# Kernel optimization log

Hardware: AMD Instinct MI355X
Metric: run time of the kernel (lower is better)

The kernel has to match this reference:

```python
import math
import jax, jax.numpy as jnp
import numpy as np
from jax.scipy.linalg import solve_triangular

K, D, Q = 512, 2048, 8
B = 8192
EPS = 1e-5
RHO0 = math.log(math.exp(1.0) - 1.0)  # softplus^-1(1.0), matches psi_init=scale_init=1.0


def setup_inputs() -> dict:
    key = jax.random.key(0)
    k1, k2, k3, k4, k5 = jax.random.split(key, 5)
    x = jax.random.normal(k1, (B, D), dtype=jnp.float32)
    mu = jax.random.normal(k2, (K, D), dtype=jnp.float32)          # centroids
    dir_raw = jax.random.normal(k3, (K, D, Q), dtype=jnp.float32) / math.sqrt(D)
    scale_rho = jnp.full((K, Q), RHO0, dtype=jnp.float32) + 0.01 * jax.random.normal(k4, (K, Q), dtype=jnp.float32)
    psi_rho = jnp.full((D,), RHO0, dtype=jnp.float32) + 0.01 * jax.random.normal(k5, (D,), dtype=jnp.float32)
    pi_logits = jnp.zeros((K,), dtype=jnp.float32)
    return {"x": x, "mu": mu, "dir_raw": dir_raw, "scale_rho": scale_rho,
            "psi_rho": psi_rho, "pi_logits": pi_logits}


def _nll(x, mu, dir_raw, scale_rho, psi_rho, pi_logits):
    Dd = x.shape[1]
    q = dir_raw.shape[2]
    # diagonal noise (shared across components since psi_per_component=False)
    psi = jax.nn.softplus(psi_rho) + EPS                      # (D,)
    psi_inv = 1.0 / psi                                       # (D,)
    # factor loadings W_k = normalize(dir_raw, dim=1) * softplus(scale)
    n = jnp.maximum(jnp.linalg.norm(dir_raw, axis=1, keepdims=True), EPS)
    W = (dir_raw / n) * jax.nn.softplus(scale_rho)[:, None, :]  # (K, D, q)
    # Woodbury inner matrix M_k = I + W^T Psi^{-1} W and its Cholesky
    A = W * jnp.sqrt(psi_inv)[None, :, None]                  # (K, D, q)
    M = jnp.einsum('kdi,kdj->kij', A, A) + jnp.eye(q, dtype=W.dtype)[None]
    L = jnp.linalg.cholesky(M)                                # (K, q, q) lower
    # quadratic form pieces
    xT_Pinv_x = (x ** 2) @ psi_inv                            # (B,)
    xT_Pinv_mu = x @ (psi_inv[None, :] * mu).T                # (B, K)
    muT_Pinv_mu = jnp.sum(mu ** 2 * psi_inv[None, :], axis=-1)  # (K,)
    quad_Psi = xT_Pinv_x[:, None] - 2.0 * xT_Pinv_mu + muT_Pinv_mu[None, :]
    PinvW = psi_inv[None, :, None] * W                        # (K, D, q)
    WT_Pinv_x = jnp.einsum('bd,kdq->bkq', x, PinvW)           # (B, K, q)
    WT_Pinv_mu = jnp.einsum('kd,kdq->kq', mu, PinvW)          # (K, q)
    v = WT_Pinv_x - WT_Pinv_mu[None, :, :]                    # (B, K, q)
    # Ez = M^{-1} v via the Cholesky factor (batched over K, rhs over B)
    vT = jnp.transpose(v, (1, 2, 0))                          # (K, q, B)
    y = solve_triangular(L, vT, lower=True)
    EzT = solve_triangular(jnp.swapaxes(L, -1, -2), y, lower=False)
    Ez = jnp.transpose(EzT, (2, 0, 1))                        # (B, K, q)
    quad = quad_Psi - jnp.sum(v * Ez, axis=-1)                # (B, K)
    # log-determinants via Woodbury: log|C| = log|Psi| + log|M|
    logdet_Psi = jnp.sum(jnp.log(psi))                        # scalar (shared psi)
    logdet_M = 2.0 * jnp.sum(jnp.log(jnp.diagonal(L, axis1=-2, axis2=-1)), axis=-1)  # (K,)
    logdet_C = logdet_Psi + logdet_M                          # (K,)
    ll = -0.5 * (Dd * math.log(2.0 * math.pi) + logdet_C[None, :] + quad)  # (B, K)
    log_pi = jax.nn.log_softmax(pi_logits)
    logp = jax.scipy.special.logsumexp(ll + log_pi[None, :], axis=1)  # (B,)
    return jnp.mean(-logp)


def reference(x, mu, dir_raw, scale_rho, psi_rho, pi_logits):
    return _nll(x, mu, dir_raw, scale_rho, psi_rho, pi_logits)
```

## Files before the change

### kernel.cpp

```cpp
#include <hip/hip_runtime.h>

constexpr int Bn = 8192;
constexpr int Dd = 2048;
constexpr int Kk = 512;
constexpr int Qq = 8;
constexpr int Nn = Kk * 9;
constexpr float DLOG2PI = 3763.9722f;

constexpr int BM = 256, BN = 144, BK = 128;

constexpr float SX = 16.f;
constexpr float SW = 64.f;
constexpr float SG = 16.f;
constexpr float INV_UW = 1.f / (16.f * 64.f);
constexpr float INV_UG = 1.f / (16.f * 16.f);

constexpr size_t OFF_PSI   = 0;
constexpr size_t OFF_LDP   = 8192;
constexpr size_t OFF_LOGPI = 8448;
constexpr size_t OFF_OFFK  = 10752;
constexpr size_t OFF_MINV  = 13056;
constexpr size_t OFF_XPX   = 144384;
constexpr size_t OFF_XBF   = 177408;
constexpr size_t OFF_GT    = 33731840;
constexpr size_t OFF_LL    = 52606208;
constexpr size_t OFF_PART  = 69383424;

typedef float f32x4 __attribute__((ext_vector_type(4)));
typedef int   i32x4v __attribute__((ext_vector_type(4)));
typedef int   i32x8v __attribute__((ext_vector_type(8)));

__device__ inline float softplusf(float x) {
  return fmaxf(x, 0.f) + log1pf(expf(-fabsf(x)));
}
__device__ inline unsigned short f2bf(float x) {
  unsigned int u = __builtin_bit_cast(unsigned int, x);
  u = (u + 0x7fffu + ((u >> 16) & 1u)) >> 16;
  return (unsigned short)u;
}
__device__ inline unsigned int pack2(float a, float b) {
  return (unsigned int)f2bf(a) | ((unsigned int)f2bf(b) << 16);
}
__device__ inline float bf2f(unsigned int u16) {
  unsigned int v = u16 << 16;
  return __builtin_bit_cast(float, v);
}
__device__ inline unsigned char f2fp8(float x) {
  int v = __builtin_amdgcn_cvt_pk_fp8_f32(x, 0.f, 0, false);
  return (unsigned char)(v & 0xff);
}
__device__ inline void glds16(const unsigned char* g, char* l) {
  __builtin_amdgcn_global_load_lds(
      (const __attribute__((address_space(1))) unsigned int*)g,
      (__attribute__((address_space(3))) unsigned int*)l, 16, 0, 0);
}
__device__ inline i32x8v ld_frag(const char* rowp, int quad, int s8) {
  i32x4v lo = *(const i32x4v*)(rowp + (((2 * quad)     ^ s8) * 16));
  i32x4v hi = *(const i32x4v*)(rowp + (((2 * quad + 1) ^ s8) * 16));
  i32x8v r;
  r[0] = lo[0]; r[1] = lo[1]; r[2] = lo[2]; r[3] = lo[3];
  r[4] = hi[0]; r[5] = hi[1]; r[6] = hi[2]; r[7] = hi[3];
  return r;
}

__global__ __launch_bounds__(256) void prep_psi(
    const float* __restrict__ psi_rho, const float* __restrict__ pi_logits,
    float* __restrict__ psi_inv, float* __restrict__ logdetPsi,
    float* __restrict__ logpi) {
  __shared__ float red[256];
  int t = threadIdx.x;
  float acc = 0.f;
  for (int d = t; d < Dd; d += 256) {
    float p = softplusf(psi_rho[d]) + 1e-5f;
    psi_inv[d] = 1.f / p;
    acc += logf(p);
  }
  red[t] = acc;
  __syncthreads();
  for (int s = 128; s > 0; s >>= 1) { if (t < s) red[t] += red[t + s]; __syncthreads(); }
  if (t == 0) *logdetPsi = red[0];
  __syncthreads();
  float mx = -3.4e38f;
  for (int i = t; i < Kk; i += 256) mx = fmaxf(mx, pi_logits[i]);
  red[t] = mx;
  __syncthreads();
  for (int s = 128; s > 0; s >>= 1) { if (t < s) red[t] = fmaxf(red[t], red[t + s]); __syncthreads(); }
  mx = red[0];
  __syncthreads();
  float se = 0.f;
  for (int i = t; i < Kk; i += 256) se += expf(pi_logits[i] - mx);
  red[t] = se;
  __syncthreads();
  for (int s = 128; s > 0; s >>= 1) { if (t < s) red[t] += red[t + s]; __syncthreads(); }
  float lse = mx + logf(red[0]);
  for (int i = t; i < Kk; i += 256) logpi[i] = pi_logits[i] - lse;
}

__global__ __launch_bounds__(256) void prep_all(
    const float* __restrict__ x, const float* __restrict__ mu,
    const float* __restrict__ dir_raw, const float* __restrict__ scale_rho,
    const float* __restrict__ psi_inv,
    float* __restrict__ offk, float* __restrict__ Minv,
    unsigned char* __restrict__ Gq, unsigned char* __restrict__ xq,
    float* __restrict__ xPx) {
  __shared__ unsigned short sDir[Dd * 8];
  __shared__ float sPwmd[Dd];
  __shared__ float redk[4 * 53];
  __shared__ float R[53];
  __shared__ float sAl[8], sAh[8];

  int bid = blockIdx.x;
  int t = threadIdx.x, lane = t & 63, w = t >> 6;

  if (bid >= Kk) {
    int b = bid - Kk;
    const float4* xr = (const float4*)(x + (size_t)b * Dd);
    const float4* pr = (const float4*)psi_inv;
    float4 v0 = xr[2 * t], v1 = xr[2 * t + 1];
    float4 p0 = pr[2 * t], p1 = pr[2 * t + 1];
    float acc = v0.x * v0.x * p0.x + v0.y * v0.y * p0.y + v0.z * v0.z * p0.z + v0.w * v0.w * p0.w
              + v1.x * v1.x * p1.x + v1.y * v1.y * p1.y + v1.z * v1.z * p1.z + v1.w * v1.w * p1.w;
    unsigned int q0 = (unsigned int)__builtin_amdgcn_cvt_pk_fp8_f32(SX * v0.x, SX * v0.y, 0, false);
    q0 = (unsigned int)__builtin_amdgcn_cvt_pk_fp8_f32(SX * v0.z, SX * v0.w, (int)q0, true);
    unsigned int q1 = (unsigned int)__builtin_amdgcn_cvt_pk_fp8_f32(SX * v1.x, SX * v1.y, 0, false);
    q1 = (unsigned int)__builtin_amdgcn_cvt_pk_fp8_f32(SX * v1.z, SX * v1.w, (int)q1, true);
    uint2 o; o.x = q0; o.y = q1;
    *(uint2*)(xq + (size_t)b * Dd + t * 8) = o;
#pragma unroll
    for (int s2 = 32; s2; s2 >>= 1) acc += __shfl_down(acc, s2, 64);
    float* r4 = sPwmd;
    if (lane == 0) r4[w] = acc;
    __syncthreads();
    if (t == 0) xPx[b] = r4[0] + r4[1] + r4[2] + r4[3];
    return;
  }

  int k = bid;
  float vals[53];
#pragma unroll
  for (int i = 0; i < 53; i++) vals[i] = 0.f;
  const float4* dirp = (const float4*)(dir_raw + (size_t)k * Dd * Qq);
  for (int d = t; d < Dd; d += 256) {
    float4 da = dirp[d * 2], db = dirp[d * 2 + 1];
    float dir8[8] = {da.x, da.y, da.z, da.w, db.x, db.y, db.z, db.w};
    float pw = psi_inv[d];
    float md = mu[(size_t)k * Dd + d];
    int c = 0;
#pragma unroll
    for (int i = 0; i < 8; i++) {
      float dip = dir8[i] * pw;
#pragma unroll
      for (int j = 0; j < 8; j++) {
        if (j < i) continue;
        vals[c] += dip * dir8[j]; c++;
      }
    }
#pragma unroll
    for (int q = 0; q < 8; q++) vals[36 + q] += dir8[q] * dir8[q];
    float mp = md * pw;
#pragma unroll
    for (int q = 0; q < 8; q++) vals[44 + q] += mp * dir8[q];
    vals[52] += md * mp;
    uint4 pk;
    pk.x = pack2(pw * dir8[0], pw * dir8[1]);
    pk.y = pack2(pw * dir8[2], pw * dir8[3]);
    pk.z = pack2(pw * dir8[4], pw * dir8[5]);
    pk.w = pack2(pw * dir8[6], pw * dir8[7]);
    *(uint4*)(sDir + d * 8) = pk;
    sPwmd[d] = mp;
  }
#pragma unroll
  for (int v = 0; v < 53; v++) {
    float val = vals[v];
#pragma unroll
    for (int o = 32; o; o >>= 1) val += __shfl_down(val, o, 64);
    if (lane == 0) redk[w * 53 + v] = val;
  }
  __syncthreads();
  if (t < 53) R[t] = redk[t] + redk[53 + t] + redk[106 + t] + redk[159 + t];
  __syncthreads();
  if (t == 0) {
    float Sf[8][8];
    {
      int c2 = 0;
#pragma unroll
      for (int i = 0; i < 8; i++) {
#pragma unroll
        for (int j = 0; j < 8; j++) {
          if (j < i) continue;
          float v = R[c2++]; Sf[i][j] = v; Sf[j][i] = v;
        }
      }
    }
    float alpha[8];
#pragma unroll
    for (int q = 0; q < 8; q++) {
      float nr = fmaxf(sqrtf(R[36 + q]), 1e-5f);
      alpha[q] = softplusf(scale_rho[(size_t)k * 8 + q]) / nr;
    }
    float Mm[8][8];
#pragma unroll
    for (int i = 0; i < 8; i++)
#pragma unroll
      for (int j = 0; j < 8; j++)
        Mm[i][j] = alpha[i] * alpha[j] * Sf[i][j] + (i == j ? 1.f : 0.f);
    float L[8][8], Ld[8];
#pragma unroll
    for (int i = 0; i < 8; i++) {
#pragma unroll
      for (int j = 0; j < 8; j++) {
        if (j > i) continue;
        float s2 = Mm[i][j];
#pragma unroll
        for (int p = 0; p < 8; p++) { if (p < j) s2 -= L[i][p] * L[j][p]; }
        if (i == j) { L[i][i] = sqrtf(s2); Ld[i] = 1.f / L[i][i]; }
        else        L[i][j] = s2 * Ld[j];
      }
    }
    float logdetM = 0.f;
#pragma unroll
    for (int i = 0; i < 8; i++) logdetM += 2.f * logf(L[i][i]);
    float wv[8];
#pragma unroll
    for (int q = 0; q < 8; q++) wv[q] = alpha[q] * R[44 + q];
    float y[8], h[8];
#pragma unroll
    for (int i = 0; i < 8; i++) {
      float s2 = wv[i];
#pragma unroll
      for (int p = 0; p < 8; p++) { if (p < i) s2 -= L[i][p] * y[p]; }
      y[i] = s2 * Ld[i];
    }
#pragma unroll
    for (int i = 7; i >= 0; i--) {
      float s2 = y[i];
#pragma unroll
      for (int p = 0; p < 8; p++) { if (p > i) s2 -= L[p][i] * h[p]; }
      h[i] = s2 * Ld[i];
    }
    float cc = R[52];
#pragma unroll
    for (int q = 0; q < 8; q++) cc -= wv[q] * h[q];
#pragma unroll
    for (int col = 0; col < 8; col++) {
      float yy[8], z[8];
#pragma unroll
      for (int i = 0; i < 8; i++) {
        float s2 = (i == col) ? 1.f : 0.f;
#pragma unroll
        for (int p = 0; p < 8; p++) { if (p < i) s2 -= L[i][p] * yy[p]; }
        yy[i] = s2 * Ld[i];
      }
#pragma unroll
      for (int i = 7; i >= 0; i--) {
        float s2 = yy[i];
#pragma unroll
        for (int p = 0; p < 8; p++) { if (p > i) s2 -= L[p][i] * z[p]; }
        z[i] = s2 * Ld[i];
      }
#pragma unroll
      for (int r2 = 0; r2 < 8; r2++) Minv[(size_t)k * 64 + r2 * 8 + col] = z[r2];
    }
    offk[k] = -0.5f * (DLOG2PI + logdetM + cc);
#pragma unroll
    for (int q = 0; q < 8; q++) { sAl[q] = alpha[q]; sAh[q] = alpha[q] * h[q]; }
  }
  __syncthreads();
  float al[8], ah[8];
#pragma unroll
  for (int q = 0; q < 8; q++) { al[q] = sAl[q]; ah[q] = sAh[q]; }
  for (int d = t; d < Dd; d += 256) {
    uint4 pk = *(const uint4*)(sDir + d * 8);
    float pd[8];
    pd[0] = bf2f(pk.x & 0xffffu); pd[1] = bf2f(pk.x >> 16);
    pd[2] = bf2f(pk.y & 0xffffu); pd[3] = bf2f(pk.y >> 16);
    pd[4] = bf2f(pk.z & 0xffffu); pd[5] = bf2f(pk.z >> 16);
    pd[6] = bf2f(pk.w & 0xffffu); pd[7] = bf2f(pk.w >> 16);
    float gs = 0.f;
#pragma unroll
    for (int q = 0; q < 8; q++) {
      Gq[((size_t)(k * 9 + q)) * Dd + d] = f2fp8(SW * al[q] * pd[q]);
      gs += ah[q] * pd[q];
    }
    Gq[((size_t)(k * 9 + 8)) * Dd + d] = f2fp8(SG * (sPwmd[d] - gs));
  }
}

__global__ __launch_bounds__(256, 2) void gemm_ll(
    const unsigned char* __restrict__ xq, const unsigned char* __restrict__ Gq,
    const float* __restrict__ Minv, const float* __restrict__ offk,
    const float* __restrict__ logpi, const float* __restrict__ logdetPsi,
    const float* __restrict__ xPx, float* __restrict__ ll) {
  __shared__ char smem[55424];
  float* Cs    = (float*)smem;
  float* sMinv = (float*)(smem + 51200);
  float* sOff  = (float*)(smem + 51200 + 4160);

  int t = threadIdx.x, lane = t & 63, w = t >> 6;
  int m0 = blockIdx.y * BM;
  int n0 = blockIdx.x * BN;
  int comp0 = blockIdx.x * 16;

  for (int i = t; i < 1024; i += 256) {
    int cl = i >> 6, idx = i & 63;
    sMinv[cl * 65 + idx] = Minv[(size_t)comp0 * 64 + i];
  }
  if (t < 16)
    sOff[t] = offk[comp0 + t] + logpi[comp0 + t] - 0.5f * logdetPsi[0];

  f32x4 acc[4][9];
  f32x4 zero = {0.f, 0.f, 0.f, 0.f};
#pragma unroll
  for (int mt = 0; mt < 4; mt++)
#pragma unroll
    for (int nt = 0; nt < 9; nt++) acc[mt][nt] = zero;

  int rr  = lane >> 3;
  int cph = lane & 7;
  int csw = cph ^ rr;
  int quad = lane >> 4, r16 = lane & 15;
  int s8 = r16 & 7;

#pragma unroll 1
  for (int k0 = 0; k0 < Dd; k0 += BK) {
    __syncthreads();
#pragma unroll
    for (int j = 0; j < 8; ++j) {
      int jj = w * 8 + j;
      glds16(xq + (size_t)(m0 + jj * 8 + rr) * Dd + k0 + csw * 16,
             smem + jj * 1024);
    }
    for (int jj = w; jj < 18; jj += 4) {
      glds16(Gq + (size_t)(n0 + jj * 8 + rr) * Dd + k0 + csw * 16,
             smem + 32768 + jj * 1024);
    }
    __syncthreads();
    i32x8v a0 = ld_frag(smem + (w * 64 +      r16) * 128, quad, s8);
    i32x8v a1 = ld_frag(smem + (w * 64 + 16 + r16) * 128, quad, s8);
    i32x8v a2 = ld_frag(smem + (w * 64 + 32 + r16) * 128, quad, s8);
    i32x8v a3 = ld_frag(smem + (w * 64 + 48 + r16) * 128, quad, s8);
#pragma unroll
    for (int nt = 0; nt < 9; ++nt) {
      i32x8v bv = ld_frag(smem + 32768 + (nt * 16 + r16) * 128, quad, s8);
      acc[0][nt] = __builtin_amdgcn_mfma_scale_f32_16x16x128_f8f6f4(
          a0, bv, acc[0][nt], 0, 0, 0, 0x7f7f7f7f, 0, 0x7f7f7f7f);
      acc[1][nt] = __builtin_amdgcn_mfma_scale_f32_16x16x128_f8f6f4(
          a1, bv, acc[1][nt], 0, 0, 0, 0x7f7f7f7f, 0, 0x7f7f7f7f);
      acc[2][nt] = __builtin_amdgcn_mfma_scale_f32_16x16x128_f8f6f4(
          a2, bv, acc[2][nt], 0, 0, 0, 0x7f7f7f7f, 0, 0x7f7f7f7f);
      acc[3][nt] = __builtin_amdgcn_mfma_scale_f32_16x16x128_f8f6f4(
          a3, bv, acc[3][nt], 0, 0, 0, 0x7f7f7f7f, 0, 0x7f7f7f7f);
    }
  }

  float P[36];
  {
    const float* Mi = sMinv + r16 * 65;
    int c = 0;
#pragma unroll
    for (int i2 = 0; i2 < 8; i2++) {
      P[c++] = 0.5f * Mi[i2 * 8 + i2];
#pragma unroll
      for (int j2 = i2 + 1; j2 < 8; j2++) P[c++] = Mi[i2 * 8 + j2];
    }
  }
  float offc = sOff[r16];

  __syncthreads();
  float* myC = Cs + w * (16 * 148);
#pragma unroll
  for (int mt = 0; mt < 4; ++mt) {
#pragma unroll
    for (int nt = 0; nt < 9; ++nt) {
#pragma unroll
      for (int r = 0; r < 4; r++) {
        myC[(quad * 4 + r) * 148 + nt * 16 + r16] = acc[mt][nt][r];
      }
    }
#pragma unroll
    for (int i = 0; i < 4; i++) {
      int row_l = quad + 4 * i;
      int b = m0 + w * 64 + mt * 16 + row_l;
      const float* cp = myC + row_l * 148 + r16 * 9;
      float u[8];
#pragma unroll
      for (int j = 0; j < 8; j++) u[j] = cp[j] * INV_UW;
      float s = cp[8] * INV_UG;
      float tq = 0.f;
      int c = 0;
#pragma unroll
      for (int i2 = 0; i2 < 8; i2++) {
        float s2 = P[c++] * u[i2];
#pragma unroll
        for (int j2 = i2 + 1; j2 < 8; j2++) s2 += P[c++] * u[j2];
        tq += u[i2] * s2;
      }
      ll[(size_t)b * Kk + comp0 + r16] = offc + s + tq - 0.5f * xPx[b];
    }
  }
}

__global__ __launch_bounds__(256) void lse_rows(
    const float* __restrict__ ll, float* __restrict__ part) {
  int t = threadIdx.x, lane = t & 63, w = t >> 6;
  int b = blockIdx.x * 4 + w;
  const float* row = ll + (size_t)b * Kk;
  float v[8];
  float mx = -3.4e38f;
#pragma unroll
  for (int i = 0; i < 8; i++) { v[i] = row[lane + 64 * i]; mx = fmaxf(mx, v[i]); }
#pragma unroll
  for (int o = 32; o; o >>= 1) mx = fmaxf(mx, __shfl_xor(mx, o, 64));
  float se = 0.f;
#pragma unroll
  for (int i = 0; i < 8; i++) se += expf(v[i] - mx);
#pragma unroll
  for (int o = 32; o; o >>= 1) se += __shfl_xor(se, o, 64);
  __shared__ float r4[4];
  if (lane == 0) r4[w] = -(mx + logf(se));
  __syncthreads();
  if (t == 0) part[blockIdx.x] = r4[0] + r4[1] + r4[2] + r4[3];
}

__global__ __launch_bounds__(256) void final_mean(
    const float* __restrict__ part, float* __restrict__ out) {
  int t = threadIdx.x, lane = t & 63, w = t >> 6;
  float acc = 0.f;
  for (int i = t; i < 2048; i += 256) acc += part[i];
#pragma unroll
  for (int o = 32; o; o >>= 1) acc += __shfl_down(acc, o, 64);
  __shared__ float r4[4];
  if (lane == 0) r4[w] = acc;
  __syncthreads();
  if (t == 0) out[0] = (r4[0] + r4[1] + r4[2] + r4[3]) * (1.0f / 8192.0f);
}

extern "C" void kernel_launch(void* const* d_in, const int* in_sizes, int n_in,
                              void* d_out, int out_size, void* d_ws, size_t ws_size,
                              hipStream_t stream) {
  const float* x         = (const float*)d_in[0];
  const float* mu        = (const float*)d_in[1];
  const float* dir_raw   = (const float*)d_in[2];
  const float* scale_rho = (const float*)d_in[3];
  const float* psi_rho   = (const float*)d_in[4];
  const float* pi_logits = (const float*)d_in[5];
  float* out = (float*)d_out;
  char* ws = (char*)d_ws;

  float* psi_inv          = (float*)(ws + OFF_PSI);
  float* logdetPsi        = (float*)(ws + OFF_LDP);
  float* logpi            = (float*)(ws + OFF_LOGPI);
  float* offk             = (float*)(ws + OFF_OFFK);
  float* Minv             = (float*)(ws + OFF_MINV);
  float* xPx              = (float*)(ws + OFF_XPX);
  unsigned char* xq       = (unsigned char*)(ws + OFF_XBF);
  unsigned char* Gq       = (unsigned char*)(ws + OFF_GT);
  float* ll               = (float*)(ws + OFF_LL);
  float* part             = (float*)(ws + OFF_PART);

  prep_psi<<<1, 256, 0, stream>>>(psi_rho, pi_logits, psi_inv, logdetPsi, logpi);
  prep_all<<<Kk + Bn, 256, 0, stream>>>(x, mu, dir_raw, scale_rho, psi_inv,
                                        offk, Minv, Gq, xq, xPx);
  dim3 g(Nn / BN, Bn / BM);
  gemm_ll<<<g, 256, 0, stream>>>(xq, Gq, Minv, offk, logpi, logdetPsi, xPx, ll);
  lse_rows<<<Bn / 4, 256, 0, stream>>>(ll, part);
  final_mean<<<1, 256, 0, stream>>>(part, out);
}
```

Measured before the change: 226.5 us.

## Double-buffer the fp8 GEMM with 8-wave 2D split and staged prefetch

Reworks gemm_ll to use 512 threads in a 4x2 wave grid and doubles the N tile so each block covers 32 components. The A and B tiles now live in a double-buffered LDS layout, which needs about 144KB of LDS. The global-to-LDS prefetch of the next K tile is split into three chunks interleaved between groups of MFMAs, with explicit vmcnt/lgkmcnt waits, barriers and s_setprio. The goal is to hide global load latency behind matrix math and reuse each A fragment across more columns. In exchange, occupancy drops to one block per CU, and the hand-written wait counts and barriers make the loop fragile.

```diff
diff --git a/kernel.cpp b/kernel.cpp
--- a/kernel.cpp
+++ b/kernel.cpp
@@ -7,7 +7,8 @@
 constexpr int Nn = Kk * 9;
 constexpr float DLOG2PI = 3763.9722f;
 
-constexpr int BM = 256, BN = 144, BK = 128;
+constexpr int BM = 256, BN = 288, BK = 128;
+constexpr int NT = Dd / BK;
 
 constexpr float SX = 16.f;
 constexpr float SW = 64.f;
@@ -26,6 +27,12 @@
 constexpr size_t OFF_LL    = 52606208;
 constexpr size_t OFF_PART  = 69383424;
 
+constexpr int LDS_AS   = 0;
+constexpr int LDS_BS   = 65536;
+constexpr int LDS_MINV = 139264;
+constexpr int LDS_OFFC = 147584;
+constexpr int LDS_TOT  = 147712;
+
 typedef float f32x4 __attribute__((ext_vector_type(4)));
 typedef int   i32x4v __attribute__((ext_vector_type(4)));
 typedef int   i32x8v __attribute__((ext_vector_type(8)));
@@ -62,6 +69,18 @@
   r[4] = hi[0]; r[5] = hi[1]; r[6] = hi[2]; r[7] = hi[3];
   return r;
 }
+
+#define BARRIER()                                   \
+  do {                                              \
+    asm volatile("" ::: "memory");                  \
+    __builtin_amdgcn_s_barrier();                   \
+    asm volatile("" ::: "memory");                  \
+  } while (0)
+#define WAITLGKM()                                  \
+  do {                                              \
+    asm volatile("s_waitcnt lgkmcnt(0)" ::: "memory"); \
+    __builtin_amdgcn_sched_barrier(0);              \
+  } while (0)
 
 __global__ __launch_bounds__(256) void prep_psi(
     const float* __restrict__ psi_rho, const float* __restrict__ pi_logits,
@@ -286,26 +305,39 @@
   }
 }
 
-__global__ __launch_bounds__(256, 2) void gemm_ll(
+#define MFMA_COL(nt, bv)                                              \
+  do {                                                                \
+    acc[0][nt] = __builtin_amdgcn_mfma_scale_f32_16x16x128_f8f6f4(    \
+        a0, bv, acc[0][nt], 0, 0, 0, 0x7f7f7f7f, 0, 0x7f7f7f7f);      \
+    acc[1][nt] = __builtin_amdgcn_mfma_scale_f32_16x16x128_f8f6f4(    \
+        a1, bv, acc[1][nt], 0, 0, 0, 0x7f7f7f7f, 0, 0x7f7f7f7f);      \
+    acc[2][nt] = __builtin_amdgcn_mfma_scale_f32_16x16x128_f8f6f4(    \
+        a2, bv, acc[2][nt], 0, 0, 0, 0x7f7f7f7f, 0, 0x7f7f7f7f);      \
+    acc[3][nt] = __builtin_amdgcn_mfma_scale_f32_16x16x128_f8f6f4(    \
+        a3, bv, acc[3][nt], 0, 0, 0, 0x7f7f7f7f, 0, 0x7f7f7f7f);      \
+  } while (0)
+
+__global__ __launch_bounds__(512, 1) void gemm_ll(
     const unsigned char* __restrict__ xq, const unsigned char* __restrict__ Gq,
     const float* __restrict__ Minv, const float* __restrict__ offk,
     const float* __restrict__ logpi, const float* __restrict__ logdetPsi,
     const float* __restrict__ xPx, float* __restrict__ ll) {
-  __shared__ char smem[55424];
+  __shared__ __align__(16) char smem[LDS_TOT];
   float* Cs    = (float*)smem;
-  float* sMinv = (float*)(smem + 51200);
-  float* sOff  = (float*)(smem + 51200 + 4160);
+  float* sMinv = (float*)(smem + LDS_MINV);
+  float* sOff  = (float*)(smem + LDS_OFFC);
 
   int t = threadIdx.x, lane = t & 63, w = t >> 6;
+  int wr = w >> 1, wc = w & 1;
   int m0 = blockIdx.y * BM;
   int n0 = blockIdx.x * BN;
-  int comp0 = blockIdx.x * 16;
-
-  for (int i = t; i < 1024; i += 256) {
+  int comp0 = blockIdx.x * 32;
+
+  for (int i = t; i < 2048; i += 512) {
     int cl = i >> 6, idx = i & 63;
     sMinv[cl * 65 + idx] = Minv[(size_t)comp0 * 64 + i];
   }
-  if (t < 16)
+  if (t < 32)
     sOff[t] = offk[comp0 + t] + logpi[comp0 + t] - 0.5f * logdetPsi[0];
 
   f32x4 acc[4][9];
@@ -320,42 +352,87 @@
   int csw = cph ^ rr;
   int quad = lane >> 4, r16 = lane & 15;
   int s8 = r16 & 7;
+  const int aoff = (wr * 64 + r16) * 128;
+  const int boff = (wc * 144 + r16) * 128;
+
+  auto stage = [&](int buf, int k0, int i0, int i1) {
+    if (w < 4) {
+      char* dst = smem + LDS_AS + buf * 32768;
+      int end = i1 > 8 ? 8 : i1;
+      for (int i = i0; i < end; ++i) {
+        int jj = w * 8 + i;
+        glds16(xq + (size_t)(m0 + jj * 8 + rr) * Dd + k0 + csw * 16,
+               dst + jj * 1024);
+      }
+    } else {
+      char* dst = smem + LDS_BS + buf * 36864;
+      for (int i = i0; i < i1; ++i) {
+        int jj = (w - 4) * 9 + i;
+        glds16(Gq + (size_t)(n0 + jj * 8 + rr) * Dd + k0 + csw * 16,
+               dst + jj * 1024);
+      }
+    }
+  };
+
+  stage(0, 0, 0, 9);
 
 #pragma unroll 1
-  for (int k0 = 0; k0 < Dd; k0 += BK) {
-    __syncthreads();
-#pragma unroll
-    for (int j = 0; j < 8; ++j) {
-      int jj = w * 8 + j;
-      glds16(xq + (size_t)(m0 + jj * 8 + rr) * Dd + k0 + csw * 16,
-             smem + jj * 1024);
-    }
-    for (int jj = w; jj < 18; jj += 4) {
-      glds16(Gq + (size_t)(n0 + jj * 8 + rr) * Dd + k0 + csw * 16,
-             smem + 32768 + jj * 1024);
-    }
-    __syncthreads();
-    i32x8v a0 = ld_frag(smem + (w * 64 +      r16) * 128, quad, s8);
-    i32x8v a1 = ld_frag(smem + (w * 64 + 16 + r16) * 128, quad, s8);
-    i32x8v a2 = ld_frag(smem + (w * 64 + 32 + r16) * 128, quad, s8);
-    i32x8v a3 = ld_frag(smem + (w * 64 + 48 + r16) * 128, quad, s8);
-#pragma unroll
-    for (int nt = 0; nt < 9; ++nt) {
-      i32x8v bv = ld_frag(smem + 32768 + (nt * 16 + r16) * 128, quad, s8);
-      acc[0][nt] = __builtin_amdgcn_mfma_scale_f32_16x16x128_f8f6f4(
-          a0, bv, acc[0][nt], 0, 0, 0, 0x7f7f7f7f, 0, 0x7f7f7f7f);
-      acc[1][nt] = __builtin_amdgcn_mfma_scale_f32_16x16x128_f8f6f4(
-          a1, bv, acc[1][nt], 0, 0, 0, 0x7f7f7f7f, 0, 0x7f7f7f7f);
-      acc[2][nt] = __builtin_amdgcn_mfma_scale_f32_16x16x128_f8f6f4(
-          a2, bv, acc[2][nt], 0, 0, 0, 0x7f7f7f7f, 0, 0x7f7f7f7f);
-      acc[3][nt] = __builtin_amdgcn_mfma_scale_f32_16x16x128_f8f6f4(
-          a3, bv, acc[3][nt], 0, 0, 0, 0x7f7f7f7f, 0, 0x7f7f7f7f);
-    }
+  for (int tt = 0; tt < NT; ++tt) {
+    int cur = tt & 1;
+    char* Ab = smem + LDS_AS + cur * 32768;
+    char* Bb = smem + LDS_BS + cur * 36864;
+    int k1 = (tt + 1) * BK;
+    if (tt < NT - 1) {
+      stage(cur ^ 1, k1, 0, 3);
+      asm volatile("s_waitcnt vmcnt(3)" ::: "memory");
+    } else {
+      asm volatile("s_waitcnt vmcnt(0)" ::: "memory");
+    }
+    BARRIER();
+    i32x8v a0 = ld_frag(Ab + aoff,        quad, s8);
+    i32x8v a1 = ld_frag(Ab + aoff + 2048, quad, s8);
+    i32x8v a2 = ld_frag(Ab + aoff + 4096, quad, s8);
+    i32x8v a3 = ld_frag(Ab + aoff + 6144, quad, s8);
+    i32x8v bv0 = ld_frag(Bb + boff,        quad, s8);
+    i32x8v bv1 = ld_frag(Bb + boff + 2048, quad, s8);
+    if (tt < NT - 1) stage(cur ^ 1, k1, 3, 6);
+    BARRIER();
+    WAITLGKM();
+    __builtin_amdgcn_s_setprio(1);
+    MFMA_COL(0, bv0);
+    MFMA_COL(1, bv1);
+    __builtin_amdgcn_s_setprio(0);
+    BARRIER();
+    i32x8v bv2 = ld_frag(Bb + boff + 2 * 2048, quad, s8);
+    i32x8v bv3 = ld_frag(Bb + boff + 3 * 2048, quad, s8);
+    i32x8v bv4 = ld_frag(Bb + boff + 4 * 2048, quad, s8);
+    if (tt < NT - 1) stage(cur ^ 1, k1, 6, 9);
+    BARRIER();
+    WAITLGKM();
+    __builtin_amdgcn_s_setprio(1);
+    MFMA_COL(2, bv2);
+    MFMA_COL(3, bv3);
+    MFMA_COL(4, bv4);
+    __builtin_amdgcn_s_setprio(0);
+    BARRIER();
+    i32x8v bv5 = ld_frag(Bb + boff + 5 * 2048, quad, s8);
+    i32x8v bv6 = ld_frag(Bb + boff + 6 * 2048, quad, s8);
+    i32x8v bv7 = ld_frag(Bb + boff + 7 * 2048, quad, s8);
+    i32x8v bv8 = ld_frag(Bb + boff + 8 * 2048, quad, s8);
+    BARRIER();
+    WAITLGKM();
+    __builtin_amdgcn_s_setprio(1);
+    MFMA_COL(5, bv5);
+    MFMA_COL(6, bv6);
+    MFMA_COL(7, bv7);
+    MFMA_COL(8, bv8);
+    __builtin_amdgcn_s_setprio(0);
+    BARRIER();
   }
 
   float P[36];
   {
-    const float* Mi = sMinv + r16 * 65;
+    const float* Mi = sMinv + (wc * 16 + r16) * 65;
     int c = 0;
 #pragma unroll
     for (int i2 = 0; i2 < 8; i2++) {
@@ -364,9 +441,8 @@
       for (int j2 = i2 + 1; j2 < 8; j2++) P[c++] = Mi[i2 * 8 + j2];
     }
   }
-  float offc = sOff[r16];
-
-  __syncthreads();
+  float offc = sOff[wc * 16 + r16];
+
   float* myC = Cs + w * (16 * 148);
 #pragma unroll
   for (int mt = 0; mt < 4; ++mt) {
@@ -380,7 +456,7 @@
 #pragma unroll
     for (int i = 0; i < 4; i++) {
       int row_l = quad + 4 * i;
-      int b = m0 + w * 64 + mt * 16 + row_l;
+      int b = m0 + wr * 64 + mt * 16 + row_l;
       const float* cp = myC + row_l * 148 + r16 * 9;
       float u[8];
 #pragma unroll
@@ -395,7 +471,7 @@
         for (int j2 = i2 + 1; j2 < 8; j2++) s2 += P[c++] * u[j2];
         tq += u[i2] * s2;
       }
-      ll[(size_t)b * Kk + comp0 + r16] = offc + s + tq - 0.5f * xPx[b];
+      ll[(size_t)b * Kk + comp0 + wc * 16 + r16] = offc + s + tq - 0.5f * xPx[b];
     }
   }
 }
@@ -462,7 +538,7 @@
   prep_all<<<Kk + Bn, 256, 0, stream>>>(x, mu, dir_raw, scale_rho, psi_inv,
                                         offk, Minv, Gq, xq, xPx);
   dim3 g(Nn / BN, Bn / BM);
-  gemm_ll<<<g, 256, 0, stream>>>(xq, Gq, Minv, offk, logpi, logdetPsi, xPx, ll);
+  gemm_ll<<<g, 512, 0, stream>>>(xq, Gq, Minv, offk, logpi, logdetPsi, xPx, ll);
   lse_rows<<<Bn / 4, 256, 0, stream>>>(ll, part);
   final_mean<<<1, 256, 0, stream>>>(part, out);
 }
```

Result: slower. 291.1 us (+28.5%).
